# Kernel optimization log

Measured on AMD Instinct MI355X. Metric: run time of the kernel, lower is better.

The kernel has to match this reference:

```python
import jax, jax.numpy as jnp
import numpy as np

# dims: batch, fast time, fast/slow embed, heads, rate, ffn hidden, pool hidden, recombine hidden
B, T, D = 2, 2048, 512
H = 8
R = 8
DS = 512
FF = 2048
HP = 2048
HR = 2048


def _ln(x, g, b):
    m = jnp.mean(x, axis=-1, keepdims=True)
    v = jnp.var(x, axis=-1, keepdims=True)
    return (x - m) / jnp.sqrt(v + 1e-5) * g + b


def _encoder_layer(x, ln1_g, ln1_b, wqkv, bqkv, wo, bo, ln2_g, ln2_b, w1, b1, w2, b2, n_heads):
    # pre-LN transformer encoder layer with causal self-attention
    b_, t, d = x.shape
    dh = d // n_heads
    h = _ln(x, ln1_g, ln1_b)
    qkv = h @ wqkv + bqkv  # [B,T,3D]
    q, k, v = jnp.split(qkv, 3, axis=-1)
    q = q.reshape(b_, t, n_heads, dh)
    k = k.reshape(b_, t, n_heads, dh)
    v = v.reshape(b_, t, n_heads, dh)
    scores = jnp.einsum('bqhd,bkhd->bhqk', q, k) / jnp.sqrt(jnp.float32(dh))
    mask = jnp.tril(jnp.ones((t, t), dtype=bool))
    scores = jnp.where(mask, scores, jnp.finfo(scores.dtype).min)
    a = jax.nn.softmax(scores, axis=-1)
    o = jnp.einsum('bhqk,bkhd->bqhd', a, v).reshape(b_, t, d)
    x = x + o @ wo + bo
    h2 = _ln(x, ln2_g, ln2_b)
    return x + jax.nn.gelu(h2 @ w1 + b1) @ w2 + b2


def _pool(f, rate, wp1, bp1, wp2, bp2):
    # causal pooling: s_k = FFN(f_{k*rate : (k+1)*rate}), prepend zero step, drop last
    b_, t, d = f.shape
    k = t // rate
    xb = f[:, :k * rate].reshape(b_, k, rate * d)  # [B,K,rate*D] block flatten
    s = jax.nn.gelu(xb @ wp1 + bp1) @ wp2 + bp2  # [B,K,DS]
    s0 = jnp.zeros((b_, 1, s.shape[-1]), s.dtype)
    return jnp.concatenate([s0, s[:, :-1]], axis=1)


def _recombine(zf, zs, rate, wr1, br1, wr2, br2):
    # lift slow to fast scale (repeat_interleave along time), concat channels, 2-layer MLP
    zl = jnp.repeat(zs, rate, axis=1)[:, :zf.shape[1]]
    x = jnp.concatenate([zf, zl], axis=-1)
    return jax.nn.gelu(x @ wr1 + br1) @ wr2 + br2


def setup_inputs() -> dict:
    key = jax.random.key(0)
    ks = iter(jax.random.split(key, 64))

    def w(shape):
        return jax.random.normal(next(ks), shape, dtype=jnp.float32) * 0.02

    def z(shape):
        return jnp.zeros(shape, dtype=jnp.float32)

    def o(shape):
        return jnp.ones(shape, dtype=jnp.float32)

    inp = {'x': jax.random.normal(next(ks), (B, T, D), dtype=jnp.float32)}
    for suf, dm, ff in (('f', D, FF), ('s', DS, FF)):
        inp['ln1' + suf + '_g'] = o((dm,)); inp['ln1' + suf + '_b'] = z((dm,))
        inp['wqkv_' + suf] = w((dm, 3 * dm)); inp['bqkv_' + suf] = z((3 * dm,))
        inp['wo_' + suf] = w((dm, dm)); inp['bo_' + suf] = z((dm,))
        inp['ln2' + suf + '_g'] = o((dm,)); inp['ln2' + suf + '_b'] = z((dm,))
        inp['w1_' + suf] = w((dm, ff)); inp['b1_' + suf] = z((ff,))
        inp['w2_' + suf] = w((ff, dm)); inp['b2_' + suf] = z((dm,))
    inp['wp1'] = w((R * D, HP)); inp['bp1'] = z((HP,))
    inp['wp2'] = w((HP, DS)); inp['bp2'] = z((DS,))
    inp['wr1'] = w((D + DS, HR)); inp['br1'] = z((HR,))
    inp['wr2'] = w((HR, D)); inp['br2'] = z((D,))
    return inp


def reference(x, ln1f_g, ln1f_b, wqkv_f, bqkv_f, wo_f, bo_f, ln2f_g, ln2f_b, w1_f, b1_f, w2_f, b2_f,
              ln1s_g, ln1s_b, wqkv_s, bqkv_s, wo_s, bo_s, ln2s_g, ln2s_b, w1_s, b1_s, w2_s, b2_s,
              wp1, bp1, wp2, bp2, wr1, br1, wr2, br2):
    # fast-scale encoder layer
    zf = _encoder_layer(x, ln1f_g, ln1f_b, wqkv_f, bqkv_f, wo_f, bo_f,
                        ln2f_g, ln2f_b, w1_f, b1_f, w2_f, b2_f, H)
    # causal pool fast -> slow
    zs_in = _pool(zf, R, wp1, bp1, wp2, bp2)
    # slow-scale encoder layer
    zs = _encoder_layer(zs_in, ln1s_g, ln1s_b, wqkv_s, bqkv_s, wo_s, bo_s,
                        ln2s_g, ln2s_b, w1_s, b1_s, w2_s, b2_s, H)
    # lift + recombine back to fast scale
    return _recombine(zf, zs, R, wr1, br1, wr2, br2)
```

## Files before the change

### kernel.cpp

```cpp
#include <hip/hip_runtime.h>
#include <cstdint>

#define DEV __device__ __forceinline__

typedef float  floatx4 __attribute__((ext_vector_type(4)));
typedef __bf16 bf16x8  __attribute__((ext_vector_type(8)));
typedef short  short8  __attribute__((ext_vector_type(8)));

DEV unsigned short f2bf(float f) {
  unsigned u = __builtin_bit_cast(unsigned, f);
  u += 0x7FFFu + ((u >> 16) & 1u);
  return (unsigned short)(u >> 16);
}
DEV float bf2f(unsigned short s) {
  unsigned u = ((unsigned)s) << 16;
  return __builtin_bit_cast(float, u);
}
DEV float gelu_f(float x) {
  float x3 = x * x * x;
  return 0.5f * x * (1.0f + tanhf(0.7978845608028654f * (x + 0.044715f * x3)));
}

DEV void stage16(const unsigned short* g, unsigned short* l) {
  __builtin_amdgcn_global_load_lds(
      (const __attribute__((address_space(1))) void*)g,
      (__attribute__((address_space(3))) void*)l, 16, 0, 0);
}

struct TrArgs {
  const float* src[12];
  unsigned short* dst[12];
  int K[12];
  int N[12];
  int off[13];
};

__global__ __launch_bounds__(256) void transpose_all_k(TrArgs a) {
  __shared__ unsigned short tile[32][33];
  int bid = blockIdx.x;
  int w = 0;
#pragma unroll
  for (int i = 0; i < 11; ++i) if (bid >= a.off[i + 1]) w = i + 1;
  int loc = bid - a.off[w];
  int tn = a.N[w] >> 5;
  int nt = (loc % tn) * 32, kt = (loc / tn) * 32;
  const float* W = a.src[w];
  unsigned short* WT = a.dst[w];
  int K = a.K[w], N = a.N[w];

  int t = threadIdx.x;
  int rr = t >> 3, c4 = (t & 7) * 4;
  const float* src = W + (size_t)(kt + rr) * N + nt + c4;
  float4 v = *reinterpret_cast<const float4*>(src);
  tile[rr][c4 + 0] = f2bf(v.x); tile[rr][c4 + 1] = f2bf(v.y);
  tile[rr][c4 + 2] = f2bf(v.z); tile[rr][c4 + 3] = f2bf(v.w);
  __syncthreads();
  unsigned short* dst = WT + (size_t)(nt + rr) * K + kt + c4;
  ushort4 o;
  o.x = tile[c4 + 0][rr]; o.y = tile[c4 + 1][rr];
  o.z = tile[c4 + 2][rr]; o.w = tile[c4 + 3][rr];
  *reinterpret_cast<ushort4*>(dst) = o;
}

__global__ void shift_k(const float* __restrict__ s, float* __restrict__ zsin) {
  int i = blockIdx.x * 256 + threadIdx.x;
  if (i >= 2 * 256 * 512) return;
  int c = i & 511, k = (i >> 9) & 255, b = i >> 17;
  zsin[i] = (k == 0) ? 0.f : s[((size_t)b * 256 + (k - 1)) * 512 + c];
}

__global__ void concat_k(const unsigned short* __restrict__ zf,
                         const unsigned short* __restrict__ zs,
                         unsigned short* __restrict__ cat) {
  int i = blockIdx.x * 256 + threadIdx.x;
  if (i >= 4096 * 1024) return;
  int c = i & 1023, rrow = i >> 10;
  int b = rrow >> 11, t = rrow & 2047;
  unsigned short v;
  if (c < 512) v = zf[(size_t)rrow * 512 + c];
  else         v = zs[((size_t)b * 256 + (t >> 3)) * 512 + (c - 512)];
  cat[i] = v;
}

template <int NP, int ACT, int RES, int OBF>
__global__ __launch_bounds__(256) void reduceN_k(const float* __restrict__ part,
                                                 const float* __restrict__ bias,
                                                 const float* __restrict__ resid,
                                                 void* __restrict__ out,
                                                 int MN, int Nmask) {
  int i = (blockIdx.x * 256 + threadIdx.x) * 4;
  if (i >= MN) return;
  float4 v = *reinterpret_cast<const float4*>(&part[i]);
#pragma unroll
  for (int p = 1; p < NP; ++p) {
    float4 t = *reinterpret_cast<const float4*>(&part[(size_t)p * MN + i]);
    v.x += t.x; v.y += t.y; v.z += t.z; v.w += t.w;
  }
  float4 bv = *reinterpret_cast<const float4*>(&bias[i & Nmask]);
  v.x += bv.x; v.y += bv.y; v.z += bv.z; v.w += bv.w;
  if (RES) {
    float4 r = *reinterpret_cast<const float4*>(&resid[i]);
    v.x += r.x; v.y += r.y; v.z += r.z; v.w += r.w;
  }
  if (ACT) { v.x = gelu_f(v.x); v.y = gelu_f(v.y); v.z = gelu_f(v.z); v.w = gelu_f(v.w); }
  if (OBF) {
    ushort4 o; o.x = f2bf(v.x); o.y = f2bf(v.y); o.z = f2bf(v.z); o.w = f2bf(v.w);
    *reinterpret_cast<ushort4*>(&((unsigned short*)out)[i]) = o;
  } else {
    *reinterpret_cast<float4*>(&((float*)out)[i]) = v;
  }
}

__global__ __launch_bounds__(64) void ln_k(const float* __restrict__ in,
                                           const float* __restrict__ g,
                                           const float* __restrict__ be,
                                           unsigned short* __restrict__ out) {
  int row = blockIdx.x, lane = threadIdx.x;
  const float* p = in + (size_t)row * 512;
  float v[8], s = 0.f, sq = 0.f;
#pragma unroll
  for (int j = 0; j < 8; ++j) { v[j] = p[j * 64 + lane]; s += v[j]; sq += v[j] * v[j]; }
#pragma unroll
  for (int off = 32; off; off >>= 1) { s += __shfl_xor(s, off, 64); sq += __shfl_xor(sq, off, 64); }
  float mean = s * (1.f / 512.f);
  float var  = sq * (1.f / 512.f) - mean * mean;
  float rstd = rsqrtf(var + 1e-5f);
#pragma unroll
  for (int j = 0; j < 8; ++j) {
    int c = j * 64 + lane;
    out[(size_t)row * 512 + c] = f2bf((v[j] - mean) * rstd * g[c] + be[c]);
  }
}

template <int TM, int ACT, int RES, int OBF, int SPLITK>
__global__ __launch_bounds__(256) void gemm_k(const unsigned short* __restrict__ A,
                                              const unsigned short* __restrict__ WT,
                                              const float* __restrict__ bias,
                                              const float* __restrict__ resid,
                                              void* __restrict__ out,
                                              int M, int K, int N) {
  constexpr int WMn = TM / 64;
  constexpr int WNn = 4 / WMn;
  constexpr int SN  = 8 / WNn;
  __shared__ __align__(16) unsigned short As[TM * 32];
  __shared__ __align__(16) unsigned short Bs[128 * 32];
  const int tid  = threadIdx.x;
  const int wv = tid >> 6, lane = tid & 63;
  const int wm = wv / WNn, wn = wv % WNn;
  const int quad = lane >> 4, l16 = lane & 15;
  const int m0 = blockIdx.y * TM, n0 = blockIdx.x * 128;
  const int sp = (SPLITK > 1) ? blockIdx.z : 0;
  const int Kc = K / SPLITK;
  const int kb0 = sp * Kc, kb1 = kb0 + Kc;

  floatx4 acc[4][SN] = {};
  const int arow = lane >> 2, acq = (lane & 3) * 8;

  for (int kb = kb0; kb < kb1; kb += 32) {
#pragma unroll
    for (int u = 0; u < WMn; ++u) {
      int g = wv * WMn + u;
      stage16(A + (size_t)(m0 + g * 16 + arow) * K + kb + acq, &As[g * 16 * 32]);
    }
#pragma unroll
    for (int u = 0; u < 2; ++u) {
      int g = wv * 2 + u;
      stage16(WT + (size_t)(n0 + g * 16 + arow) * K + kb + acq, &Bs[g * 16 * 32]);
    }
    __syncthreads();
    bf16x8 af[4], bfr[SN];
#pragma unroll
    for (int i = 0; i < 4; ++i)
      af[i] = *reinterpret_cast<const bf16x8*>(&As[(wm * 64 + i * 16 + l16) * 32 + quad * 8]);
#pragma unroll
    for (int j = 0; j < SN; ++j)
      bfr[j] = *reinterpret_cast<const bf16x8*>(&Bs[(wn * (SN * 16) + j * 16 + l16) * 32 + quad * 8]);
#pragma unroll
    for (int i = 0; i < 4; ++i)
#pragma unroll
      for (int j = 0; j < SN; ++j)
        acc[i][j] = __builtin_amdgcn_mfma_f32_16x16x32_bf16(af[i], bfr[j], acc[i][j], 0, 0, 0);
    __syncthreads();
  }

#pragma unroll
  for (int i = 0; i < 4; ++i) {
    int row_base = m0 + wm * 64 + i * 16 + quad * 4;
#pragma unroll
    for (int j = 0; j < SN; ++j) {
      int col = n0 + wn * (SN * 16) + j * 16 + l16;
      float bv = (SPLITK > 1) ? 0.f : bias[col];
#pragma unroll
      for (int rr = 0; rr < 4; ++rr) {
        int row = row_base + rr;
        float v = acc[i][j][rr];
        if (SPLITK > 1) {
          ((float*)out)[((size_t)sp * M + row) * N + col] = v;
        } else {
          v += bv;
          if (RES) v += resid[(size_t)row * N + col];
          if (ACT) v = gelu_f(v);
          if (OBF) ((unsigned short*)out)[(size_t)row * N + col] = f2bf(v);
          else     ((float*)out)[(size_t)row * N + col] = v;
        }
      }
    }
  }
}

__global__ __launch_bounds__(256) void attn_k(const unsigned short* __restrict__ qkv,
                                              unsigned short* __restrict__ out, int T) {
  const int ld = 1536, Dm = 512;
  __shared__ unsigned short Ks[2][64 * 72];
  __shared__ unsigned short Vt[2][64 * 72];
  __shared__ unsigned short ps[4][16 * 72];
  const int tid = threadIdx.x, wv = tid >> 6, lane = tid & 63;
  const int quad = lane >> 4, l16 = lane & 15;
  const int nqt = T >> 6;
  const int z = blockIdx.x;
  const int bh = z & 15;
  const int qt = nqt - 1 - (z >> 4);
  const int b = bh >> 3, hh = bh & 7;
  const int q0 = qt * 64 + wv * 16;
  const size_t bT = (size_t)b * T;

  const unsigned short* qp = qkv + (bT + q0 + l16) * ld + hh * 64 + quad * 8;
  short8 qa = *reinterpret_cast<const short8*>(qp);
  short8 qb = *reinterpret_cast<const short8*>(qp + 32);
  unsigned short qs0[8] __attribute__((aligned(16)));
  unsigned short qs1[8] __attribute__((aligned(16)));
#pragma unroll
  for (int u = 0; u < 8; ++u) {
    qs0[u] = f2bf(bf2f((unsigned short)qa[u]) * 0.125f);
    qs1[u] = f2bf(bf2f((unsigned short)qb[u]) * 0.125f);
  }
  bf16x8 aq0 = *reinterpret_cast<const bf16x8*>(qs0);
  bf16x8 aq1 = *reinterpret_cast<const bf16x8*>(qs1);

  floatx4 O[4] = {};
  float l_r[4] = {0.f, 0.f, 0.f, 0.f};

  const int nch = qt + 1;
  const int skey = tid >> 2, scc = (tid & 3) * 16;
  const int vkey = (tid & 31) * 2, vdg = tid >> 5;

  short8 kA, kB, vA, vB;
  auto prefetch = [&](int c) {
    const unsigned short* kp = qkv + (bT + c * 64 + skey) * ld + Dm + hh * 64 + scc;
    kA = *reinterpret_cast<const short8*>(kp);
    kB = *reinterpret_cast<const short8*>(kp + 8);
    const unsigned short* vp = qkv + (bT + c * 64 + vkey) * ld + 1024 + hh * 64 + vdg * 8;
    vA = *reinterpret_cast<const short8*>(vp);
    vB = *reinterpret_cast<const short8*>(vp + ld);
  };
  auto stage = [&](int buf) {
    *reinterpret_cast<short8*>(&Ks[buf][skey * 72 + scc])     = kA;
    *reinterpret_cast<short8*>(&Ks[buf][skey * 72 + scc + 8]) = kB;
#pragma unroll
    for (int u = 0; u < 8; ++u) {
      unsigned pk = ((unsigned)(unsigned short)vB[u] << 16) | (unsigned short)vA[u];
      *reinterpret_cast<unsigned*>(&Vt[buf][(vdg * 8 + u) * 72 + vkey]) = pk;
    }
  };

  prefetch(0);
  stage(0);
  __syncthreads();

  for (int c = 0; c < nch; ++c) {
    const int buf = c & 1;
    const bool last = (c == nch - 1);
    if (!last) prefetch(c + 1);

    floatx4 S[4];
#pragma unroll
    for (int sub = 0; sub < 4; ++sub) {
      const unsigned short* kr = &Ks[buf][(sub * 16 + l16) * 72 + quad * 8];
      bf16x8 b0 = *reinterpret_cast<const bf16x8*>(kr);
      bf16x8 b1 = *reinterpret_cast<const bf16x8*>(kr + 32);
      floatx4 sacc = {};
      sacc = __builtin_amdgcn_mfma_f32_16x16x32_bf16(aq0, b0, sacc, 0, 0, 0);
      sacc = __builtin_amdgcn_mfma_f32_16x16x32_bf16(aq1, b1, sacc, 0, 0, 0);
      S[sub] = sacc;
    }

    if (last) {
      const int k0 = c * 64;
#pragma unroll
      for (int r = 0; r < 4; ++r) {
        int qg = q0 + quad * 4 + r;
#pragma unroll
        for (int sub = 0; sub < 4; ++sub) {
          int kg = k0 + sub * 16 + l16;
          if (kg > qg) S[sub][r] = -3.0e38f;
        }
      }
    }
#pragma unroll
    for (int sub = 0; sub < 4; ++sub)
#pragma unroll
      for (int r = 0; r < 4; ++r) {
        float p = __expf(S[sub][r]);
        S[sub][r] = p;
        l_r[r] += p;
      }

#pragma unroll
    for (int sub = 0; sub < 4; ++sub)
#pragma unroll
      for (int r = 0; r < 4; ++r)
        ps[wv][(quad * 4 + r) * 72 + sub * 16 + l16] = f2bf(S[sub][r]);
    bf16x8 p0 = *reinterpret_cast<const bf16x8*>(&ps[wv][l16 * 72 + quad * 8]);
    bf16x8 p1 = *reinterpret_cast<const bf16x8*>(&ps[wv][l16 * 72 + 32 + quad * 8]);

#pragma unroll
    for (int sd = 0; sd < 4; ++sd) {
      const unsigned short* vr = &Vt[buf][(sd * 16 + l16) * 72 + quad * 8];
      bf16x8 v0 = *reinterpret_cast<const bf16x8*>(vr);
      bf16x8 v1 = *reinterpret_cast<const bf16x8*>(vr + 32);
      O[sd] = __builtin_amdgcn_mfma_f32_16x16x32_bf16(p0, v0, O[sd], 0, 0, 0);
      O[sd] = __builtin_amdgcn_mfma_f32_16x16x32_bf16(p1, v1, O[sd], 0, 0, 0);
    }

    if (!last) stage((c + 1) & 1);
    __syncthreads();
  }

#pragma unroll
  for (int r = 0; r < 4; ++r) {
    float l = l_r[r];
    l += __shfl_xor(l, 1, 64);
    l += __shfl_xor(l, 2, 64);
    l += __shfl_xor(l, 4, 64);
    l += __shfl_xor(l, 8, 64);
    l_r[r] = l;
  }

#pragma unroll
  for (int sd = 0; sd < 4; ++sd)
#pragma unroll
    for (int r = 0; r < 4; ++r) {
      int qg = q0 + quad * 4 + r;
      out[(bT + qg) * Dm + hh * 64 + sd * 16 + l16] = f2bf(O[sd][r] / l_r[r]);
    }
}

extern "C" void kernel_launch(void* const* d_in, const int* in_sizes, int n_in,
                              void* d_out, int out_size, void* d_ws, size_t ws_size,
                              hipStream_t stream) {
  (void)in_sizes; (void)n_in; (void)out_size; (void)ws_size;
  const int B = 2, T = 2048, FF = 2048, HP = 2048, HR = 2048;
  const int BT = B * T;
  const int BK = B * 256;

  const float* x      = (const float*)d_in[0];
  const float* ln1f_g = (const float*)d_in[1];
  const float* ln1f_b = (const float*)d_in[2];
  const float* wqkv_f = (const float*)d_in[3];
  const float* bqkv_f = (const float*)d_in[4];
  const float* wo_f   = (const float*)d_in[5];
  const float* bo_f   = (const float*)d_in[6];
  const float* ln2f_g = (const float*)d_in[7];
  const float* ln2f_b = (const float*)d_in[8];
  const float* w1_f   = (const float*)d_in[9];
  const float* b1_f   = (const float*)d_in[10];
  const float* w2_f   = (const float*)d_in[11];
  const float* b2_f   = (const float*)d_in[12];
  const float* ln1s_g = (const float*)d_in[13];
  const float* ln1s_b = (const float*)d_in[14];
  const float* wqkv_s = (const float*)d_in[15];
  const float* bqkv_s = (const float*)d_in[16];
  const float* wo_s   = (const float*)d_in[17];
  const float* bo_s   = (const float*)d_in[18];
  const float* ln2s_g = (const float*)d_in[19];
  const float* ln2s_b = (const float*)d_in[20];
  const float* w1_s   = (const float*)d_in[21];
  const float* b1_s   = (const float*)d_in[22];
  const float* w2_s   = (const float*)d_in[23];
  const float* b2_s   = (const float*)d_in[24];
  const float* wp1    = (const float*)d_in[25];
  const float* bp1    = (const float*)d_in[26];
  const float* wp2    = (const float*)d_in[27];
  const float* bp2    = (const float*)d_in[28];
  const float* wr1    = (const float*)d_in[29];
  const float* br1    = (const float*)d_in[30];
  const float* wr2    = (const float*)d_in[31];
  const float* br2    = (const float*)d_in[32];

  char* ws = (char*)d_ws;
  const size_t HMB = 512 * 1024;
  unsigned short* wtbase = (unsigned short*)(ws);
  unsigned short* h      = (unsigned short*)(ws + 76  * HMB);
  unsigned short* qkv    = (unsigned short*)(ws + 84  * HMB);
  unsigned short* attn   = (unsigned short*)(ws + 108 * HMB);
  float*          x1     = (float*)(ws + 116 * HMB);
  unsigned short* mid    = (unsigned short*)(ws + 132 * HMB);
  unsigned short* zf     = (unsigned short*)(ws + 164 * HMB);
  unsigned short* pmid   = (unsigned short*)(ws + 84  * HMB);
  float*          spool  = (float*)(ws + 88  * HMB);
  float*          zsin   = (float*)(ws + 90  * HMB);
  unsigned short* sh     = (unsigned short*)(ws + 92  * HMB);
  unsigned short* sqkv   = (unsigned short*)(ws + 93  * HMB);
  unsigned short* sattn  = (unsigned short*)(ws + 96  * HMB);
  float*          sx1    = (float*)(ws + 97  * HMB);
  unsigned short* smid   = (unsigned short*)(ws + 99  * HMB);
  unsigned short* szs    = (unsigned short*)(ws + 103 * HMB);
  float*          part   = (float*)(ws + 172 * HMB);
  unsigned short* cat    = (unsigned short*)(ws + 240 * HMB);
  unsigned short* mid2   = (unsigned short*)(ws + 256 * HMB);

  size_t wo_off = 0;
  auto walloc = [&](size_t n) { unsigned short* p = wtbase + wo_off; wo_off += n; return p; };
  unsigned short* t_qkv_f = walloc((size_t)512 * 1536);
  unsigned short* t_wo_f  = walloc((size_t)512 * 512);
  unsigned short* t_w1_f  = walloc((size_t)512 * 2048);
  unsigned short* t_w2_f  = walloc((size_t)2048 * 512);
  unsigned short* t_qkv_s = walloc((size_t)512 * 1536);
  unsigned short* t_wo_s  = walloc((size_t)512 * 512);
  unsigned short* t_w1_s  = walloc((size_t)512 * 2048);
  unsigned short* t_w2_s  = walloc((size_t)2048 * 512);
  unsigned short* t_wp1   = walloc((size_t)4096 * 2048);
  unsigned short* t_wp2   = walloc((size_t)2048 * 512);
  unsigned short* t_wr1   = walloc((size_t)1024 * 2048);
  unsigned short* t_wr2   = walloc((size_t)2048 * 512);

  {
    TrArgs a;
    const float* srcs[12] = {wqkv_f, wo_f, w1_f, w2_f, wqkv_s, wo_s, w1_s, w2_s,
                             wp1, wp2, wr1, wr2};
    unsigned short* dsts[12] = {t_qkv_f, t_wo_f, t_w1_f, t_w2_f, t_qkv_s, t_wo_s,
                                t_w1_s, t_w2_s, t_wp1, t_wp2, t_wr1, t_wr2};
    int Ks[12] = {512, 512, 512, 2048, 512, 512, 512, 2048, 4096, 2048, 1024, 2048};
    int Ns[12] = {1536, 512, 2048, 512, 1536, 512, 2048, 512, 2048, 512, 2048, 512};
    int off = 0;
    for (int i = 0; i < 12; ++i) {
      a.src[i] = srcs[i]; a.dst[i] = dsts[i]; a.K[i] = Ks[i]; a.N[i] = Ns[i];
      a.off[i] = off;
      off += (Ks[i] / 32) * (Ns[i] / 32);
    }
    a.off[12] = off;
    transpose_all_k<<<off, 256, 0, stream>>>(a);
  }

  ln_k<<<BT, 64, 0, stream>>>(x, ln1f_g, ln1f_b, h);
  gemm_k<64, 0, 0, 1, 1><<<dim3(12, 64), 256, 0, stream>>>(h, t_qkv_f, bqkv_f, nullptr, qkv, BT, 512, 1536);
  attn_k<<<(T / 64) * 16, 256, 0, stream>>>(qkv, attn, T);
  gemm_k<64, 0, 0, 0, 2><<<dim3(4, 64, 2), 256, 0, stream>>>(attn, t_wo_f, nullptr, nullptr, part, BT, 512, 512);
  reduceN_k<2, 0, 1, 0><<<(BT * 512) / 1024, 256, 0, stream>>>(part, bo_f, x, x1, BT * 512, 511);
  ln_k<<<BT, 64, 0, stream>>>(x1, ln2f_g, ln2f_b, h);
  gemm_k<128, 1, 0, 1, 1><<<dim3(16, 32), 256, 0, stream>>>(h, t_w1_f, b1_f, nullptr, mid, BT, 512, FF);
  gemm_k<64, 0, 0, 0, 2><<<dim3(4, 64, 2), 256, 0, stream>>>(mid, t_w2_f, nullptr, nullptr, part, BT, FF, 512);
  reduceN_k<2, 0, 1, 1><<<(BT * 512) / 1024, 256, 0, stream>>>(part, b2_f, x1, zf, BT * 512, 511);

  gemm_k<128, 0, 0, 0, 8><<<dim3(16, 4, 8), 256, 0, stream>>>(zf, t_wp1, nullptr, nullptr, part, BK, 4096, HP);
  reduceN_k<8, 1, 0, 1><<<(BK * HP) / 1024, 256, 0, stream>>>(part, bp1, nullptr, pmid, BK * HP, HP - 1);
  gemm_k<64, 0, 0, 0, 4><<<dim3(4, 8, 4), 256, 0, stream>>>(pmid, t_wp2, nullptr, nullptr, part, BK, HP, 512);
  reduceN_k<4, 0, 0, 0><<<(BK * 512) / 1024, 256, 0, stream>>>(part, bp2, nullptr, spool, BK * 512, 511);
  shift_k<<<(BK * 512) / 256, 256, 0, stream>>>(spool, zsin);

  ln_k<<<BK, 64, 0, stream>>>(zsin, ln1s_g, ln1s_b, sh);
  gemm_k<64, 0, 0, 1, 1><<<dim3(12, 8), 256, 0, stream>>>(sh, t_qkv_s, bqkv_s, nullptr, sqkv, BK, 512, 1536);
  attn_k<<<(256 / 64) * 16, 256, 0, stream>>>(sqkv, sattn, 256);
  gemm_k<64, 0, 1, 0, 1><<<dim3(4, 8), 256, 0, stream>>>(sattn, t_wo_s, bo_s, zsin, sx1, BK, 512, 512);
  ln_k<<<BK, 64, 0, stream>>>(sx1, ln2s_g, ln2s_b, sh);
  gemm_k<64, 1, 0, 1, 1><<<dim3(16, 8), 256, 0, stream>>>(sh, t_w1_s, b1_s, nullptr, smid, BK, 512, FF);
  gemm_k<64, 0, 1, 1, 1><<<dim3(4, 8), 256, 0, stream>>>(smid, t_w2_s, b2_s, sx1, szs, BK, FF, 512);

  concat_k<<<(BT * 1024) / 256, 256, 0, stream>>>(zf, szs, cat);
  gemm_k<128, 1, 0, 1, 1><<<dim3(16, 32), 256, 0, stream>>>(cat, t_wr1, br1, nullptr, mid2, BT, 1024, HR);
  gemm_k<64, 0, 0, 0, 2><<<dim3(4, 64, 2), 256, 0, stream>>>(mid2, t_wr2, nullptr, nullptr, part, BT, HR, 512);
  reduceN_k<2, 0, 0, 0><<<(BT * 512) / 1024, 256, 0, stream>>>(part, br2, nullptr, d_out, BT * 512, 511);
}
```

Before: 503.9 us.

## Double-buffer GEMM LDS tiles with K=64 steps and XOR-swizzled layout

The GEMM main loop now stages each A/B tile into one of two LDS buffers, issuing the next tile's global-to-LDS loads before computing on the current one. This should overlap memory latency with MFMA work and halve the barriers per K. The K step grows from 32 to 64, and the LDS layout is XOR-swizzled to avoid bank conflicts on fragment reads. LDS use doubles or more, which may reduce occupancy. K must now be a multiple of 64 per split.

```diff
diff --git a/kernel.cpp b/kernel.cpp
--- a/kernel.cpp
+++ b/kernel.cpp
@@ -142,8 +142,9 @@
   constexpr int WMn = TM / 64;
   constexpr int WNn = 4 / WMn;
   constexpr int SN  = 8 / WNn;
-  __shared__ __align__(16) unsigned short As[TM * 32];
-  __shared__ __align__(16) unsigned short Bs[128 * 32];
+  constexpr int APW = TM / 32;
+  __shared__ __align__(16) unsigned short As[2][TM * 64];
+  __shared__ __align__(16) unsigned short Bs[2][128 * 64];
   const int tid  = threadIdx.x;
   const int wv = tid >> 6, lane = tid & 63;
   const int wm = wv / WNn, wn = wv % WNn;
@@ -151,35 +152,57 @@
   const int m0 = blockIdx.y * TM, n0 = blockIdx.x * 128;
   const int sp = (SPLITK > 1) ? blockIdx.z : 0;
   const int Kc = K / SPLITK;
-  const int kb0 = sp * Kc, kb1 = kb0 + Kc;
+  const int kb0 = sp * Kc;
+  const int nk = Kc / 64;
+  const int lrow = lane >> 3;
+  const int scol = ((lane & 7) ^ lrow) * 8;
+  const int sx = l16 & 7;
 
   floatx4 acc[4][SN] = {};
-  const int arow = lane >> 2, acq = (lane & 3) * 8;
-
-  for (int kb = kb0; kb < kb1; kb += 32) {
-#pragma unroll
-    for (int u = 0; u < WMn; ++u) {
-      int g = wv * WMn + u;
-      stage16(A + (size_t)(m0 + g * 16 + arow) * K + kb + acq, &As[g * 16 * 32]);
-    }
-#pragma unroll
-    for (int u = 0; u < 2; ++u) {
-      int g = wv * 2 + u;
-      stage16(WT + (size_t)(n0 + g * 16 + arow) * K + kb + acq, &Bs[g * 16 * 32]);
-    }
-    __syncthreads();
-    bf16x8 af[4], bfr[SN];
+
+  auto stage = [&](int buf, int kb) {
+#pragma unroll
+    for (int u = 0; u < APW; ++u) {
+      int g = wv * APW + u;
+      stage16(A + (size_t)(m0 + g * 8 + lrow) * K + kb + scol, &As[buf][g * 512]);
+    }
+#pragma unroll
+    for (int u = 0; u < 4; ++u) {
+      int g = wv * 4 + u;
+      stage16(WT + (size_t)(n0 + g * 8 + lrow) * K + kb + scol, &Bs[buf][g * 512]);
+    }
+  };
+
+  stage(0, kb0);
+  __syncthreads();
+
+  for (int t = 0; t < nk; ++t) {
+    const int buf = t & 1;
+    if (t + 1 < nk) stage(buf ^ 1, kb0 + (t + 1) * 64);
+    bf16x8 af[4][2], bfr[SN][2];
+#pragma unroll
+    for (int i = 0; i < 4; ++i) {
+      const int r = wm * 64 + i * 16 + l16;
+#pragma unroll
+      for (int kk = 0; kk < 2; ++kk)
+        af[i][kk] = *reinterpret_cast<const bf16x8*>(
+            &As[buf][r * 64 + (((kk * 4 + quad) ^ sx) * 8)]);
+    }
+#pragma unroll
+    for (int j = 0; j < SN; ++j) {
+      const int r = wn * (SN * 16) + j * 16 + l16;
+#pragma unroll
+      for (int kk = 0; kk < 2; ++kk)
+        bfr[j][kk] = *reinterpret_cast<const bf16x8*>(
+            &Bs[buf][r * 64 + (((kk * 4 + quad) ^ sx) * 8)]);
+    }
 #pragma unroll
     for (int i = 0; i < 4; ++i)
-      af[i] = *reinterpret_cast<const bf16x8*>(&As[(wm * 64 + i * 16 + l16) * 32 + quad * 8]);
-#pragma unroll
-    for (int j = 0; j < SN; ++j)
-      bfr[j] = *reinterpret_cast<const bf16x8*>(&Bs[(wn * (SN * 16) + j * 16 + l16) * 32 + quad * 8]);
-#pragma unroll
-    for (int i = 0; i < 4; ++i)
-#pragma unroll
-      for (int j = 0; j < SN; ++j)
-        acc[i][j] = __builtin_amdgcn_mfma_f32_16x16x32_bf16(af[i], bfr[j], acc[i][j], 0, 0, 0);
+#pragma unroll
+      for (int j = 0; j < SN; ++j) {
+        acc[i][j] = __builtin_amdgcn_mfma_f32_16x16x32_bf16(af[i][0], bfr[j][0], acc[i][j], 0, 0, 0);
+        acc[i][j] = __builtin_amdgcn_mfma_f32_16x16x32_bf16(af[i][1], bfr[j][1], acc[i][j], 0, 0, 0);
+      }
     __syncthreads();
   }
 
```

New measurement: 451.1 us. 1.12x faster.
